# Kernel optimization log

Measured on AMD Instinct MI355X. Metric: run time of the kernel, lower is better.

Reference implementation:

```python
import jax, jax.numpy as jnp
import numpy as np

N = 100000
E = 3200000
F_IN = 128
HID = 128
NC = 10
G = 512  # number of graphs in batch


def setup_inputs() -> dict:
    key = jax.random.key(0)
    ks = jax.random.split(key, 9)
    x = jax.random.normal(ks[0], (N, F_IN), dtype=jnp.float32)
    edge_index = jax.random.randint(ks[1], (2, E), 0, N, dtype=jnp.int64)
    batch = jnp.sort(jax.random.randint(ks[2], (N,), 0, G, dtype=jnp.int64))
    s = 1.0 / np.sqrt(F_IN)
    W1 = jax.random.uniform(ks[3], (F_IN, HID), jnp.float32, -s, s)
    b1 = jnp.zeros((HID,), jnp.float32)
    sh = 1.0 / np.sqrt(HID)
    W2 = jax.random.uniform(ks[4], (HID, HID), jnp.float32, -sh, sh)
    b2 = jnp.zeros((HID,), jnp.float32)
    Wc = jax.random.uniform(ks[5], (HID, NC), jnp.float32, -sh, sh)
    bc = jax.random.uniform(ks[6], (NC,), jnp.float32, -sh, sh)
    return {"x": x, "edge_index": edge_index, "batch": batch,
            "W1": W1, "b1": b1, "W2": W2, "b2": b2, "Wc": Wc, "bc": bc}


def _gcn_conv(x, src, dst, norm, W, b):
    # linear transform first (PyG GCNConv), then normalized scatter-add
    h = x @ W                              # [N, H]
    msg = h[src] * norm[:, None]           # gather + scale, [E+N, H]
    out = jax.ops.segment_sum(msg, dst, num_segments=N)
    return out + b


def reference(x, edge_index, batch, W1, b1, W2, b2, Wc, bc):
    # add self-loops (PyG gcn_norm default)
    loop = jnp.arange(N, dtype=edge_index.dtype)
    src = jnp.concatenate([edge_index[0], loop])
    dst = jnp.concatenate([edge_index[1], loop])
    deg = jax.ops.segment_sum(jnp.ones_like(dst, dtype=x.dtype), dst, num_segments=N)
    dis = jnp.where(deg > 0, jax.lax.rsqrt(deg), 0.0)  # deg^{-1/2}
    norm = dis[src] * dis[dst]

    h = jax.nn.relu(_gcn_conv(x, src, dst, norm, W1, b1))
    # dropout is identity in eval mode
    h = jax.nn.relu(_gcn_conv(h, src, dst, norm, W2, b2))

    # global mean pool over graph ids
    sums = jax.ops.segment_sum(h, batch, num_segments=G)
    cnts = jax.ops.segment_sum(jnp.ones((N,), h.dtype), batch, num_segments=G)
    pooled = sums / jnp.maximum(cnts, 1.0)[:, None]   # [G, HID]

    logits = pooled @ Wc + bc                          # [G, NC]
    return logits, pooled
```

## Files before the change

### kernel.cpp

```cpp
#include <hip/hip_runtime.h>
#include <hip/hip_bf16.h>

typedef short bf16x8 __attribute__((ext_vector_type(8)));
typedef float f32x4 __attribute__((ext_vector_type(4)));
typedef unsigned int u32x4 __attribute__((ext_vector_type(4)));

__device__ __forceinline__ unsigned short f2bf(float f) {
    unsigned int u = __float_as_uint(f);
    unsigned int r = u + 0x7fffu + ((u >> 16) & 1u);
    return (unsigned short)(r >> 16);
}
__device__ __forceinline__ float bf2f(unsigned short b) {
    return __uint_as_float(((unsigned int)b) << 16);
}
__device__ __forceinline__ unsigned int packbf2(float lo, float hi) {
    return ((unsigned int)f2bf(hi) << 16) | (unsigned int)f2bf(lo);
}

__global__ __launch_bounds__(256) void hist_k(const int* __restrict__ dst, int* __restrict__ hist,
                                              const float* __restrict__ W1, const float* __restrict__ W2,
                                              unsigned short* __restrict__ wt1, unsigned short* __restrict__ wt2,
                                              int e, int nbuk, int nblk, int eb) {
    int blk = blockIdx.x, t = threadIdx.x;
    if (blk >= nblk) {
        int j = (blk - nblk) * 256 + t;
        int k = j >> 7, nn = j & 127;
        wt1[nn * 128 + k] = f2bf(W1[j]);
        wt2[nn * 128 + k] = f2bf(W2[j]);
        return;
    }
    __shared__ int lh[512];
    for (int j = t; j < nbuk; j += 256) lh[j] = 0;
    __syncthreads();
    int e0 = blk * eb, e1 = min(e, e0 + eb);
    for (int i = e0 + t; i < e1; i += 256) atomicAdd(&lh[dst[i] >> 8], 1);
    __syncthreads();
    for (int j = t; j < nbuk; j += 256) hist[(size_t)j * nblk + blk] = lh[j];
}

__global__ __launch_bounds__(256) void scanA_k(int* __restrict__ hist, int* __restrict__ btot, int nbuk, int nblk) {
    int w = (blockIdx.x * 256 + threadIdx.x) >> 6;
    int lane = threadIdx.x & 63;
    if (w >= nbuk) return;
    size_t base = (size_t)w * nblk;
    int run = 0;
    for (int c = 0; c < nblk; c += 64) {
        int i = c + lane;
        int v = (i < nblk) ? hist[base + i] : 0;
        int orig = v;
        for (int d = 1; d < 64; d <<= 1) { int u = __shfl_up(v, d); if (lane >= d) v += u; }
        if (i < nblk) hist[base + i] = run + v - orig;
        run += __shfl(v, 63);
    }
    if (lane == 0) btot[w] = run;
}

__global__ __launch_bounds__(512) void scanB_k(const int* __restrict__ btot, int* __restrict__ bbase, int nbuk) {
    __shared__ int s[512];
    int t = threadIdx.x;
    int v = (t < nbuk) ? btot[t] : 0;
    s[t] = v;
    __syncthreads();
    for (int st = 1; st < 512; st <<= 1) {
        int add = (t >= st) ? s[t - st] : 0;
        __syncthreads();
        s[t] += add;
        __syncthreads();
    }
    if (t < nbuk) bbase[t] = s[t] - v;
    if (t == nbuk - 1) bbase[nbuk] = s[t];
}

__global__ __launch_bounds__(256) void scatter_k(const int* __restrict__ src, const int* __restrict__ dst,
                                                 const int* __restrict__ hist, const int* __restrict__ bbase,
                                                 unsigned int* __restrict__ coarse, int e, int nbuk, int nblk, int eb) {
    __shared__ int cur[512];
    int blk = blockIdx.x, t = threadIdx.x;
    for (int j = t; j < nbuk; j += 256) cur[j] = bbase[j] + hist[(size_t)j * nblk + blk];
    __syncthreads();
    int e0 = blk * eb, e1 = min(e, e0 + eb);
    for (int i = e0 + t; i < e1; i += 256) {
        int s = src[i], d = dst[i];
        int bk = d >> 8;
        int p = atomicAdd(&cur[bk], 1);
        coarse[p] = ((unsigned int)(d & 255) << 24) | (unsigned int)s;
    }
}

__global__ __launch_bounds__(256) void bucket_k(const unsigned int* __restrict__ coarse, const int* __restrict__ bbase,
                                                float* __restrict__ dis, int* __restrict__ row_ptr, int* __restrict__ col,
                                                int n, int nbuk, int e) {
    __shared__ int h[256];
    __shared__ int s[256];
    __shared__ int cur[256];
    int b = blockIdx.x, t = threadIdx.x;
    int e0 = bbase[b], e1 = bbase[b + 1];
    h[t] = 0;
    __syncthreads();
    for (int i = e0 + t; i < e1; i += 256) atomicAdd(&h[coarse[i] >> 24], 1);
    __syncthreads();
    int v = h[t];
    s[t] = v;
    __syncthreads();
    for (int st = 1; st < 256; st <<= 1) {
        int add = (t >= st) ? s[t - st] : 0;
        __syncthreads();
        s[t] += add;
        __syncthreads();
    }
    int excl = s[t] - v;
    int node = b * 256 + t;
    if (node < n) {
        row_ptr[node] = e0 + excl;
        dis[node] = rsqrtf((float)v + 1.0f);
    }
    cur[t] = e0 + excl;
    __syncthreads();
    for (int i = e0 + t; i < e1; i += 256) {
        unsigned int pk = coarse[i];
        int p = atomicAdd(&cur[pk >> 24], 1);
        col[p] = (int)(pk & 0x00FFFFFFu);
    }
    if (b == nbuk - 1 && t == 0) row_ptr[n] = e;
}

template <bool INF32>
__global__ __launch_bounds__(256) void gemm_mfma_k(const void* __restrict__ Av, const unsigned short* __restrict__ WTg,
                                                   const float* __restrict__ dis, unsigned short* __restrict__ C,
                                                   int nrows) {
    __shared__ __align__(16) unsigned short WT[128 * 136];
    int t = threadIdx.x;
#pragma unroll
    for (int i = t; i < 2048; i += 256) {
        int nn = i >> 4, c = i & 15;
        *(u32x4*)&WT[nn * 136 + c * 8] = *(const u32x4*)&WTg[nn * 128 + c * 8];
    }
    __syncthreads();
    int wave = t >> 6, lane = t & 63;
    int lm = lane & 15, lg = lane >> 4;
    for (int m0 = blockIdx.x * 64; m0 < nrows; m0 += gridDim.x * 64) {
        int R = m0 + wave * 16;
        int arow = R + lm;
        if (arow >= nrows) arow = nrows - 1;
        f32x4 acc[8];
#pragma unroll
        for (int q = 0; q < 8; q++) acc[q] = (f32x4){0.f, 0.f, 0.f, 0.f};
#pragma unroll
        for (int kk = 0; kk < 4; kk++) {
            bf16x8 af;
            if constexpr (INF32) {
                const float4* ap = (const float4*)((const float*)Av + (size_t)arow * 128 + kk * 32 + lg * 8);
                float4 a0 = ap[0], a1 = ap[1];
                u32x4 au;
                au[0] = packbf2(a0.x, a0.y); au[1] = packbf2(a0.z, a0.w);
                au[2] = packbf2(a1.x, a1.y); au[3] = packbf2(a1.z, a1.w);
                af = __builtin_bit_cast(bf16x8, au);
            } else {
                const u32x4* ap = (const u32x4*)((const unsigned short*)Av + (size_t)arow * 128);
                af = __builtin_bit_cast(bf16x8, ap[kk * 4 + lg]);
            }
#pragma unroll
            for (int q = 0; q < 8; q++) {
                const u32x4* bp = (const u32x4*)(WT + (q * 16 + lm) * 136 + kk * 32 + lg * 8);
                bf16x8 bfr = __builtin_bit_cast(bf16x8, *bp);
                acc[q] = __builtin_amdgcn_mfma_f32_16x16x32_bf16(af, bfr, acc[q], 0, 0, 0);
            }
        }
        float dsc[4];
#pragma unroll
        for (int i2 = 0; i2 < 4; i2++) {
            int r = R + lg * 4 + i2;
            dsc[i2] = (r < nrows) ? dis[r] : 0.f;
        }
#pragma unroll
        for (int i2 = 0; i2 < 4; i2++) {
            int r = R + lg * 4 + i2;
            if (r < nrows) {
                unsigned short* cp = C + (size_t)r * 128 + lm;
#pragma unroll
                for (int q = 0; q < 8; q++) cp[q * 16] = f2bf(acc[q][i2] * dsc[i2]);
            }
        }
    }
}

__global__ __launch_bounds__(256, 8) void agg_k(const unsigned short* __restrict__ h, unsigned short* __restrict__ out,
                                                const int* __restrict__ row_ptr, const int* __restrict__ col,
                                                const float* __restrict__ dis, const float* __restrict__ bias, int n) {
    int wid  = (blockIdx.x * 256 + threadIdx.x) >> 6;
    int lane = threadIdx.x & 63;
    if (wid >= n) return;
    int g = lane >> 4;
    int s = lane & 15;
    const char* hb = (const char*)h;
    unsigned int soff = (unsigned int)(s << 4);
    float acc0 = 0.f, acc1 = 0.f, acc2 = 0.f, acc3 = 0.f;
    float acc4 = 0.f, acc5 = 0.f, acc6 = 0.f, acc7 = 0.f;
#define ACCUM(v)                                                                              \
    acc0 += __uint_as_float((v)[0] << 16); acc1 += __uint_as_float((v)[0] & 0xffff0000u);     \
    acc2 += __uint_as_float((v)[1] << 16); acc3 += __uint_as_float((v)[1] & 0xffff0000u);     \
    acc4 += __uint_as_float((v)[2] << 16); acc5 += __uint_as_float((v)[2] & 0xffff0000u);     \
    acc6 += __uint_as_float((v)[3] << 16); acc7 += __uint_as_float((v)[3] & 0xffff0000u);
    if (g == 0) {
        u32x4 v = *(const u32x4*)(hb + (((unsigned int)wid << 8) + soff));
        ACCUM(v)
    }
    int e = row_ptr[wid] + g, e1 = row_ptr[wid + 1];
    for (; e + 12 < e1; e += 16) {
        int c0 = col[e], c1 = col[e + 4], c2 = col[e + 8], c3 = col[e + 12];
        u32x4 v0 = *(const u32x4*)(hb + (((unsigned int)c0 << 8) + soff));
        u32x4 v1 = *(const u32x4*)(hb + (((unsigned int)c1 << 8) + soff));
        u32x4 v2 = *(const u32x4*)(hb + (((unsigned int)c2 << 8) + soff));
        u32x4 v3 = *(const u32x4*)(hb + (((unsigned int)c3 << 8) + soff));
        ACCUM(v0)
        ACCUM(v1)
        ACCUM(v2)
        ACCUM(v3)
    }
    for (; e < e1; e += 4) {
        u32x4 v = *(const u32x4*)(hb + (((unsigned int)col[e] << 8) + soff));
        ACCUM(v)
    }
#undef ACCUM
#define RED(a) a += __shfl_xor(a, 16); a += __shfl_xor(a, 32);
    RED(acc0) RED(acc1) RED(acc2) RED(acc3) RED(acc4) RED(acc5) RED(acc6) RED(acc7)
#undef RED
    if (g == 0) {
        float d = dis[wid];
        const float4* bp = (const float4*)bias;
        float4 ba = bp[2 * s], bb = bp[2 * s + 1];
        u32x4 r;
        r[0] = packbf2(fmaxf(ba.x + d * acc0, 0.f), fmaxf(ba.y + d * acc1, 0.f));
        r[1] = packbf2(fmaxf(ba.z + d * acc2, 0.f), fmaxf(ba.w + d * acc3, 0.f));
        r[2] = packbf2(fmaxf(bb.x + d * acc4, 0.f), fmaxf(bb.y + d * acc5, 0.f));
        r[3] = packbf2(fmaxf(bb.z + d * acc6, 0.f), fmaxf(bb.w + d * acc7, 0.f));
        *(u32x4*)((char*)out + (((unsigned int)wid << 8) + soff)) = r;
    }
}

__global__ __launch_bounds__(128) void pool_logits_k(const unsigned short* __restrict__ h, const int* __restrict__ batch,
                                                     const float* __restrict__ Wc, const float* __restrict__ bc,
                                                     float* __restrict__ logits, float* __restrict__ pooled,
                                                     int n, int nc) {
    __shared__ float pl[128];
    int g = blockIdx.x;
    int j = threadIdx.x;
    int lo = 0, hi = n;
    while (lo < hi) { int mid = (lo + hi) >> 1; if (batch[mid] < g) lo = mid + 1; else hi = mid; }
    int start = lo;
    hi = n;
    while (lo < hi) { int mid = (lo + hi) >> 1; if (batch[mid] < g + 1) lo = mid + 1; else hi = mid; }
    int end = lo;
    float acc = 0.f;
    for (int r = start; r < end; r++) acc += bf2f(h[(size_t)r * 128 + j]);
    float pv = acc / fmaxf((float)(end - start), 1.0f);
    pooled[(size_t)g * 128 + j] = pv;
    pl[j] = pv;
    __syncthreads();
    if (j < nc) {
        float a = bc[j];
#pragma unroll 8
        for (int k = 0; k < 128; k++) a += pl[k] * Wc[k * nc + j];
        logits[(size_t)g * nc + j] = a;
    }
}

extern "C" void kernel_launch(void* const* d_in, const int* in_sizes, int n_in,
                              void* d_out, int out_size, void* d_ws, size_t ws_size,
                              hipStream_t stream) {
    const float* x     = (const float*)d_in[0];
    const int*   ei    = (const int*)d_in[1];
    const int*   batch = (const int*)d_in[2];
    const float* W1    = (const float*)d_in[3];
    const float* b1    = (const float*)d_in[4];
    const float* W2    = (const float*)d_in[5];
    const float* b2    = (const float*)d_in[6];
    const float* Wc    = (const float*)d_in[7];
    const float* bc    = (const float*)d_in[8];
    float* out = (float*)d_out;

    const int N = in_sizes[0] / 128;
    const int E = in_sizes[1] / 2;
    const int NC = 10;
    const int G = out_size / (NC + 128);

    const int* src = ei;
    const int* dst = ei + E;

    const int EB   = 8192;
    const int NBLK = (E + EB - 1) / EB;
    const int NBUK = (N + 255) / 256;

    char* wbase = (char*)d_ws;
    size_t off = 0;
    auto alloc = [&](size_t bytes) -> void* {
        void* p = wbase + off;
        off = (off + bytes + 255) & ~(size_t)255;
        return p;
    };
    float* dis     = (float*)alloc((size_t)N * 4);
    int*   row_ptr = (int*)alloc((size_t)(N + 1) * 4);
    int*   hist    = (int*)alloc((size_t)NBUK * NBLK * 4);
    int*   btot    = (int*)alloc((size_t)NBUK * 4);
    int*   bbase   = (int*)alloc((size_t)(NBUK + 1) * 4);
    unsigned int* coarse = (unsigned int*)alloc((size_t)E * 4);
    int*   col     = (int*)alloc((size_t)E * 4);
    unsigned short* wt1 = (unsigned short*)alloc((size_t)128 * 128 * 2);
    unsigned short* wt2 = (unsigned short*)alloc((size_t)128 * 128 * 2);
    unsigned short* bufT = (unsigned short*)alloc((size_t)N * 128 * 2);
    unsigned short* bufH = (unsigned short*)alloc((size_t)N * 128 * 2);

    hist_k<<<NBLK + 64, 256, 0, stream>>>(dst, hist, W1, W2, wt1, wt2, E, NBUK, NBLK, EB);
    scanA_k<<<(NBUK * 64 + 255) / 256, 256, 0, stream>>>(hist, btot, NBUK, NBLK);
    scanB_k<<<1, 512, 0, stream>>>(btot, bbase, NBUK);
    scatter_k<<<NBLK, 256, 0, stream>>>(src, dst, hist, bbase, coarse, E, NBUK, NBLK, EB);
    bucket_k<<<NBUK, 256, 0, stream>>>(coarse, bbase, dis, row_ptr, col, N, NBUK, E);

    const int gemmBlocks = (N + 63) / 64;
    gemm_mfma_k<true><<<gemmBlocks, 256, 0, stream>>>(x, wt1, dis, bufT, N);
    agg_k<<<(N + 3) / 4, 256, 0, stream>>>(bufT, bufH, row_ptr, col, dis, b1, N);
    gemm_mfma_k<false><<<gemmBlocks, 256, 0, stream>>>(bufH, wt2, dis, bufT, N);
    agg_k<<<(N + 3) / 4, 256, 0, stream>>>(bufT, bufH, row_ptr, col, dis, b2, N);

    float* pooled = out + (size_t)G * NC;
    pool_logits_k<<<G, 128, 0, stream>>>(bufH, batch, Wc, bc, out, pooled, N, NC);
}
```

Baseline: 403.6 us.

## Fuse first GEMM into histogram kernel and fold bucket scan into consumers

The layer-1 GEMM (x@W1, unscaled) now runs inside the histogram kernel as extra blocks, so it can overlap with edge counting instead of waiting for the degree normalization. The first aggregation then applies the per-source dis factor per edge by gathering dis[col]. The separate single-block bucket scan kernel is removed and each scatter/bucket block recomputes the 391-entry prefix itself. Histogram and scatter loops also switch to int4 vector loads. The trade-offs are an extra per-edge dis gather in the first aggregation and redundant small scans in every block.

```diff
diff --git a/kernel.cpp b/kernel.cpp
--- a/kernel.cpp
+++ b/kernel.cpp
@@ -17,25 +17,77 @@
     return ((unsigned int)f2bf(hi) << 16) | (unsigned int)f2bf(lo);
 }
 
-__global__ __launch_bounds__(256) void hist_k(const int* __restrict__ dst, int* __restrict__ hist,
-                                              const float* __restrict__ W1, const float* __restrict__ W2,
-                                              unsigned short* __restrict__ wt1, unsigned short* __restrict__ wt2,
-                                              int e, int nbuk, int nblk, int eb) {
+__global__ __launch_bounds__(256) void build1_k(const int* __restrict__ dst, int* __restrict__ hist,
+                                                const float* __restrict__ W1, const float* __restrict__ W2,
+                                                unsigned short* __restrict__ wt2,
+                                                const float* __restrict__ x, unsigned short* __restrict__ T,
+                                                int nrows, int e, int nbuk, int nblk, int eb, int g1) {
+    __shared__ int lh[512];
+    __shared__ __align__(16) unsigned short WT[128 * 136];
     int blk = blockIdx.x, t = threadIdx.x;
-    if (blk >= nblk) {
+    if (blk < nblk) {
+        for (int j = t; j < nbuk; j += 256) lh[j] = 0;
+        __syncthreads();
+        int e0 = blk * eb, e1 = min(e, e0 + eb);
+        int L = e1 - e0;
+        int i = e0 + t * 4;
+        for (; i + 3 < e1; i += 1024) {
+            int4 d4 = *(const int4*)(dst + i);
+            atomicAdd(&lh[d4.x >> 8], 1);
+            atomicAdd(&lh[d4.y >> 8], 1);
+            atomicAdd(&lh[d4.z >> 8], 1);
+            atomicAdd(&lh[d4.w >> 8], 1);
+        }
+        int rem = L & 3;
+        if (t < rem) atomicAdd(&lh[dst[e1 - rem + t] >> 8], 1);
+        __syncthreads();
+        for (int j = t; j < nbuk; j += 256) hist[(size_t)j * nblk + blk] = lh[j];
+    } else if (blk < nblk + 64) {
         int j = (blk - nblk) * 256 + t;
         int k = j >> 7, nn = j & 127;
-        wt1[nn * 128 + k] = f2bf(W1[j]);
         wt2[nn * 128 + k] = f2bf(W2[j]);
-        return;
-    }
-    __shared__ int lh[512];
-    for (int j = t; j < nbuk; j += 256) lh[j] = 0;
-    __syncthreads();
-    int e0 = blk * eb, e1 = min(e, e0 + eb);
-    for (int i = e0 + t; i < e1; i += 256) atomicAdd(&lh[dst[i] >> 8], 1);
-    __syncthreads();
-    for (int j = t; j < nbuk; j += 256) hist[(size_t)j * nblk + blk] = lh[j];
+    } else {
+        int bid = blk - nblk - 64;
+        for (int i = t; i < 16384; i += 256) {
+            int k = i >> 7, nn = i & 127;
+            WT[nn * 136 + k] = f2bf(W1[i]);
+        }
+        __syncthreads();
+        int wave = t >> 6, lane = t & 63;
+        int lm = lane & 15, lg = lane >> 4;
+        for (int m0 = bid * 64; m0 < nrows; m0 += g1 * 64) {
+            int R = m0 + wave * 16;
+            int arow = R + lm;
+            if (arow >= nrows) arow = nrows - 1;
+            f32x4 acc[8];
+#pragma unroll
+            for (int q = 0; q < 8; q++) acc[q] = (f32x4){0.f, 0.f, 0.f, 0.f};
+#pragma unroll
+            for (int kk = 0; kk < 4; kk++) {
+                const float4* ap = (const float4*)(x + (size_t)arow * 128 + kk * 32 + lg * 8);
+                float4 a0 = ap[0], a1 = ap[1];
+                u32x4 au;
+                au[0] = packbf2(a0.x, a0.y); au[1] = packbf2(a0.z, a0.w);
+                au[2] = packbf2(a1.x, a1.y); au[3] = packbf2(a1.z, a1.w);
+                bf16x8 af = __builtin_bit_cast(bf16x8, au);
+#pragma unroll
+                for (int q = 0; q < 8; q++) {
+                    const u32x4* bp = (const u32x4*)(WT + (q * 16 + lm) * 136 + kk * 32 + lg * 8);
+                    bf16x8 bfr = __builtin_bit_cast(bf16x8, *bp);
+                    acc[q] = __builtin_amdgcn_mfma_f32_16x16x32_bf16(af, bfr, acc[q], 0, 0, 0);
+                }
+            }
+#pragma unroll
+            for (int i2 = 0; i2 < 4; i2++) {
+                int r = R + lg * 4 + i2;
+                if (r < nrows) {
+                    unsigned short* cp = T + (size_t)r * 128 + lm;
+#pragma unroll
+                    for (int q = 0; q < 8; q++) cp[q * 16] = f2bf(acc[q][i2]);
+                }
+            }
+        }
+    }
 }
 
 __global__ __launch_bounds__(256) void scanA_k(int* __restrict__ hist, int* __restrict__ btot, int nbuk, int nblk) {
@@ -55,48 +107,75 @@
     if (lane == 0) btot[w] = run;
 }
 
-__global__ __launch_bounds__(512) void scanB_k(const int* __restrict__ btot, int* __restrict__ bbase, int nbuk) {
-    __shared__ int s[512];
-    int t = threadIdx.x;
-    int v = (t < nbuk) ? btot[t] : 0;
-    s[t] = v;
-    __syncthreads();
-    for (int st = 1; st < 512; st <<= 1) {
-        int add = (t >= st) ? s[t - st] : 0;
-        __syncthreads();
-        s[t] += add;
-        __syncthreads();
-    }
-    if (t < nbuk) bbase[t] = s[t] - v;
-    if (t == nbuk - 1) bbase[nbuk] = s[t];
-}
-
 __global__ __launch_bounds__(256) void scatter_k(const int* __restrict__ src, const int* __restrict__ dst,
-                                                 const int* __restrict__ hist, const int* __restrict__ bbase,
+                                                 const int* __restrict__ hist, const int* __restrict__ btot,
                                                  unsigned int* __restrict__ coarse, int e, int nbuk, int nblk, int eb) {
+    __shared__ int lbase[512];
     __shared__ int cur[512];
     int blk = blockIdx.x, t = threadIdx.x;
-    for (int j = t; j < nbuk; j += 256) cur[j] = bbase[j] + hist[(size_t)j * nblk + blk];
+    int wv = t >> 6, lane = t & 63;
+    if (wv == 0) {
+        int run = 0;
+        for (int c = 0; c < nbuk; c += 64) {
+            int i = c + lane;
+            int v = (i < nbuk) ? btot[i] : 0;
+            int orig = v;
+            for (int d = 1; d < 64; d <<= 1) { int u = __shfl_up(v, d); if (lane >= d) v += u; }
+            if (i < nbuk) lbase[i] = run + v - orig;
+            run += __shfl(v, 63);
+        }
+    }
+    __syncthreads();
+    for (int j = t; j < nbuk; j += 256) cur[j] = lbase[j] + hist[(size_t)j * nblk + blk];
     __syncthreads();
     int e0 = blk * eb, e1 = min(e, e0 + eb);
-    for (int i = e0 + t; i < e1; i += 256) {
-        int s = src[i], d = dst[i];
-        int bk = d >> 8;
-        int p = atomicAdd(&cur[bk], 1);
+    int L = e1 - e0;
+    int i = e0 + t * 4;
+    for (; i + 3 < e1; i += 1024) {
+        int4 s4 = *(const int4*)(src + i);
+        int4 d4 = *(const int4*)(dst + i);
+        int p0 = atomicAdd(&cur[d4.x >> 8], 1);
+        coarse[p0] = ((unsigned int)(d4.x & 255) << 24) | (unsigned int)s4.x;
+        int p1 = atomicAdd(&cur[d4.y >> 8], 1);
+        coarse[p1] = ((unsigned int)(d4.y & 255) << 24) | (unsigned int)s4.y;
+        int p2 = atomicAdd(&cur[d4.z >> 8], 1);
+        coarse[p2] = ((unsigned int)(d4.z & 255) << 24) | (unsigned int)s4.z;
+        int p3 = atomicAdd(&cur[d4.w >> 8], 1);
+        coarse[p3] = ((unsigned int)(d4.w & 255) << 24) | (unsigned int)s4.w;
+    }
+    int rem = L & 3;
+    if (t < rem) {
+        int idx = e1 - rem + t;
+        int s = src[idx], d = dst[idx];
+        int p = atomicAdd(&cur[d >> 8], 1);
         coarse[p] = ((unsigned int)(d & 255) << 24) | (unsigned int)s;
     }
 }
 
-__global__ __launch_bounds__(256) void bucket_k(const unsigned int* __restrict__ coarse, const int* __restrict__ bbase,
+__global__ __launch_bounds__(256) void bucket_k(const unsigned int* __restrict__ coarse, const int* __restrict__ btot,
                                                 float* __restrict__ dis, int* __restrict__ row_ptr, int* __restrict__ col,
                                                 int n, int nbuk, int e) {
+    __shared__ int lbase[512];
     __shared__ int h[256];
     __shared__ int s[256];
     __shared__ int cur[256];
     int b = blockIdx.x, t = threadIdx.x;
-    int e0 = bbase[b], e1 = bbase[b + 1];
+    int wv = t >> 6, lane = t & 63;
+    if (wv == 0) {
+        int run = 0;
+        for (int c = 0; c < nbuk; c += 64) {
+            int i = c + lane;
+            int v = (i < nbuk) ? btot[i] : 0;
+            int orig = v;
+            for (int d = 1; d < 64; d <<= 1) { int u = __shfl_up(v, d); if (lane >= d) v += u; }
+            if (i < nbuk) lbase[i] = run + v - orig;
+            run += __shfl(v, 63);
+        }
+        if (lane == 0) lbase[nbuk] = run;
+    }
     h[t] = 0;
     __syncthreads();
+    int e0 = lbase[b], e1 = lbase[b + 1];
     for (int i = e0 + t; i < e1; i += 256) atomicAdd(&h[coarse[i] >> 24], 1);
     __syncthreads();
     int v = h[t];
@@ -184,6 +263,7 @@
     }
 }
 
+template <bool EDGE_DIS>
 __global__ __launch_bounds__(256, 8) void agg_k(const unsigned short* __restrict__ h, unsigned short* __restrict__ out,
                                                 const int* __restrict__ row_ptr, const int* __restrict__ col,
                                                 const float* __restrict__ dis, const float* __restrict__ bias, int n) {
@@ -194,46 +274,52 @@
     int s = lane & 15;
     const char* hb = (const char*)h;
     unsigned int soff = (unsigned int)(s << 4);
+    float dn = dis[wid];
     float acc0 = 0.f, acc1 = 0.f, acc2 = 0.f, acc3 = 0.f;
     float acc4 = 0.f, acc5 = 0.f, acc6 = 0.f, acc7 = 0.f;
-#define ACCUM(v)                                                                              \
-    acc0 += __uint_as_float((v)[0] << 16); acc1 += __uint_as_float((v)[0] & 0xffff0000u);     \
-    acc2 += __uint_as_float((v)[1] << 16); acc3 += __uint_as_float((v)[1] & 0xffff0000u);     \
-    acc4 += __uint_as_float((v)[2] << 16); acc5 += __uint_as_float((v)[2] & 0xffff0000u);     \
-    acc6 += __uint_as_float((v)[3] << 16); acc7 += __uint_as_float((v)[3] & 0xffff0000u);
+#define ACCUMW(v, w)                                                                                  \
+    acc0 += (w) * __uint_as_float((v)[0] << 16); acc1 += (w) * __uint_as_float((v)[0] & 0xffff0000u); \
+    acc2 += (w) * __uint_as_float((v)[1] << 16); acc3 += (w) * __uint_as_float((v)[1] & 0xffff0000u); \
+    acc4 += (w) * __uint_as_float((v)[2] << 16); acc5 += (w) * __uint_as_float((v)[2] & 0xffff0000u); \
+    acc6 += (w) * __uint_as_float((v)[3] << 16); acc7 += (w) * __uint_as_float((v)[3] & 0xffff0000u);
     if (g == 0) {
         u32x4 v = *(const u32x4*)(hb + (((unsigned int)wid << 8) + soff));
-        ACCUM(v)
+        float w = EDGE_DIS ? dn : 1.0f;
+        ACCUMW(v, w)
     }
     int e = row_ptr[wid] + g, e1 = row_ptr[wid + 1];
     for (; e + 12 < e1; e += 16) {
         int c0 = col[e], c1 = col[e + 4], c2 = col[e + 8], c3 = col[e + 12];
+        float w0 = 1.f, w1 = 1.f, w2 = 1.f, w3 = 1.f;
+        if constexpr (EDGE_DIS) { w0 = dis[c0]; w1 = dis[c1]; w2 = dis[c2]; w3 = dis[c3]; }
         u32x4 v0 = *(const u32x4*)(hb + (((unsigned int)c0 << 8) + soff));
         u32x4 v1 = *(const u32x4*)(hb + (((unsigned int)c1 << 8) + soff));
         u32x4 v2 = *(const u32x4*)(hb + (((unsigned int)c2 << 8) + soff));
         u32x4 v3 = *(const u32x4*)(hb + (((unsigned int)c3 << 8) + soff));
-        ACCUM(v0)
-        ACCUM(v1)
-        ACCUM(v2)
-        ACCUM(v3)
+        ACCUMW(v0, w0)
+        ACCUMW(v1, w1)
+        ACCUMW(v2, w2)
+        ACCUMW(v3, w3)
     }
     for (; e < e1; e += 4) {
-        u32x4 v = *(const u32x4*)(hb + (((unsigned int)col[e] << 8) + soff));
-        ACCUM(v)
-    }
-#undef ACCUM
+        int c = col[e];
+        float w = 1.f;
+        if constexpr (EDGE_DIS) w = dis[c];
+        u32x4 v = *(const u32x4*)(hb + (((unsigned int)c << 8) + soff));
+        ACCUMW(v, w)
+    }
+#undef ACCUMW
 #define RED(a) a += __shfl_xor(a, 16); a += __shfl_xor(a, 32);
     RED(acc0) RED(acc1) RED(acc2) RED(acc3) RED(acc4) RED(acc5) RED(acc6) RED(acc7)
 #undef RED
     if (g == 0) {
-        float d = dis[wid];
         const float4* bp = (const float4*)bias;
         float4 ba = bp[2 * s], bb = bp[2 * s + 1];
         u32x4 r;
-        r[0] = packbf2(fmaxf(ba.x + d * acc0, 0.f), fmaxf(ba.y + d * acc1, 0.f));
-        r[1] = packbf2(fmaxf(ba.z + d * acc2, 0.f), fmaxf(ba.w + d * acc3, 0.f));
-        r[2] = packbf2(fmaxf(bb.x + d * acc4, 0.f), fmaxf(bb.y + d * acc5, 0.f));
-        r[3] = packbf2(fmaxf(bb.z + d * acc6, 0.f), fmaxf(bb.w + d * acc7, 0.f));
+        r[0] = packbf2(fmaxf(ba.x + dn * acc0, 0.f), fmaxf(ba.y + dn * acc1, 0.f));
+        r[1] = packbf2(fmaxf(ba.z + dn * acc2, 0.f), fmaxf(ba.w + dn * acc3, 0.f));
+        r[2] = packbf2(fmaxf(bb.x + dn * acc4, 0.f), fmaxf(bb.y + dn * acc5, 0.f));
+        r[3] = packbf2(fmaxf(bb.z + dn * acc6, 0.f), fmaxf(bb.w + dn * acc7, 0.f));
         *(u32x4*)((char*)out + (((unsigned int)wid << 8) + soff)) = r;
     }
 }
@@ -302,25 +388,21 @@
     int*   row_ptr = (int*)alloc((size_t)(N + 1) * 4);
     int*   hist    = (int*)alloc((size_t)NBUK * NBLK * 4);
     int*   btot    = (int*)alloc((size_t)NBUK * 4);
-    int*   bbase   = (int*)alloc((size_t)(NBUK + 1) * 4);
     unsigned int* coarse = (unsigned int*)alloc((size_t)E * 4);
     int*   col     = (int*)alloc((size_t)E * 4);
-    unsigned short* wt1 = (unsigned short*)alloc((size_t)128 * 128 * 2);
     unsigned short* wt2 = (unsigned short*)alloc((size_t)128 * 128 * 2);
     unsigned short* bufT = (unsigned short*)alloc((size_t)N * 128 * 2);
     unsigned short* bufH = (unsigned short*)alloc((size_t)N * 128 * 2);
 
-    hist_k<<<NBLK + 64, 256, 0, stream>>>(dst, hist, W1, W2, wt1, wt2, E, NBUK, NBLK, EB);
+    const int G1 = 782;
+    build1_k<<<NBLK + 64 + G1, 256, 0, stream>>>(dst, hist, W1, W2, wt2, x, bufT, N, E, NBUK, NBLK, EB, G1);
     scanA_k<<<(NBUK * 64 + 255) / 256, 256, 0, stream>>>(hist, btot, NBUK, NBLK);
-    scanB_k<<<1, 512, 0, stream>>>(btot, bbase, NBUK);
-    scatter_k<<<NBLK, 256, 0, stream>>>(src, dst, hist, bbase, coarse, E, NBUK, NBLK, EB);
-    bucket_k<<<NBUK, 256, 0, stream>>>(coarse, bbase, dis, row_ptr, col, N, NBUK, E);
-
-    const int gemmBlocks = (N + 63) / 64;
-    gemm_mfma_k<true><<<gemmBlocks, 256, 0, stream>>>(x, wt1, dis, bufT, N);
-    agg_k<<<(N + 3) / 4, 256, 0, stream>>>(bufT, bufH, row_ptr, col, dis, b1, N);
-    gemm_mfma_k<false><<<gemmBlocks, 256, 0, stream>>>(bufH, wt2, dis, bufT, N);
-    agg_k<<<(N + 3) / 4, 256, 0, stream>>>(bufT, bufH, row_ptr, col, dis, b2, N);
+    scatter_k<<<NBLK, 256, 0, stream>>>(src, dst, hist, btot, coarse, E, NBUK, NBLK, EB);
+    bucket_k<<<NBUK, 256, 0, stream>>>(coarse, btot, dis, row_ptr, col, N, NBUK, E);
+
+    agg_k<true><<<(N + 3) / 4, 256, 0, stream>>>(bufT, bufH, row_ptr, col, dis, b1, N);
+    gemm_mfma_k<false><<<(N + 63) / 64, 256, 0, stream>>>(bufH, wt2, dis, bufT, N);
+    agg_k<false><<<(N + 3) / 4, 256, 0, stream>>>(bufT, bufH, row_ptr, col, dis, b2, N);
 
     float* pooled = out + (size_t)G * NC;
     pool_logits_k<<<G, 128, 0, stream>>>(bufH, batch, Wc, bc, out, pooled, N, NC);
```

Measured after the change: 395.6 us. 1.02x faster.
